# Kernel tuning notes

Measured on AMD Instinct MI355X. Metric: run time of the kernel, lower is better.

The kernel has to match this reference:

```python
import jax, jax.numpy as jnp
import numpy as np

B, U, D, SKIP = 2048, 1024, 1024, 24

def setup_inputs() -> dict:
    key = jax.random.key(0)
    ks = jax.random.split(key, 8)
    return {
        "inputs": jax.random.normal(ks[0], (B, D), dtype=jnp.float32),
        "h_tm1": jax.random.normal(ks[1], (B, 4 * U), dtype=jnp.float32),
        "c_tm1": jax.random.normal(ks[2], (B, U), dtype=jnp.float32),
        "step": jnp.zeros((B, 1), dtype=jnp.float32),
        "prev_h": jax.random.normal(ks[3], (B, U * SKIP), dtype=jnp.float32),
        "kernel": jax.random.normal(ks[4], (D, 4 * U), dtype=jnp.float32) * (1.0 / np.sqrt(D)),
        "recurrent_kernel": jax.random.normal(ks[5], (U, 4 * U), dtype=jnp.float32) * (1.0 / np.sqrt(U)),
        "kernel2": jax.random.normal(ks[6], (U, U), dtype=jnp.float32) * (1.0 / np.sqrt(U)),
        "bias": jnp.zeros((4 * U,), dtype=jnp.float32),
        "bias2": jnp.zeros((U,), dtype=jnp.float32),
        "s0": jnp.float32(0.5),
    }

def reference(inputs, h_tm1, c_tm1, step, prev_h, kernel, recurrent_kernel, kernel2, bias, bias2, s0):
    units = kernel2.shape[0]
    # split previous 'h' state into its four gate-history blocks [B, U] each
    h_parts = jnp.stack(jnp.split(h_tm1, 4, axis=1), axis=0)          # [4, B, U]
    rk = recurrent_kernel.reshape(units, 4, units)                     # [U, 4, U]
    # fused per-gate recurrent matmuls: r[g] = h_parts[g] @ recurrent_kernel[:, g*U:(g+1)*U]
    r = jnp.einsum('gbu,ugv->gbv', h_parts, rk)                        # [4, B, U]
    x = inputs @ kernel + bias                                         # [B, 4U]
    x_i, x_f, x_c, x_o = jnp.split(x, 4, axis=1)
    i = jax.nn.sigmoid(x_i + r[0])
    f = jax.nn.sigmoid(x_f + r[1])
    c = f * c_tm1 + i * jnp.tanh(x_c + r[2])
    o = jax.nn.sigmoid(x_o + r[3])
    h = o * jnp.tanh(c)
    new_h_skip = jax.nn.sigmoid(prev_h[:, :units] @ kernel2 + bias2)
    h = s0 * h + new_h_skip * (1 - s0)
    new_h_tm1 = jnp.concatenate([i, f, c, o], axis=1)
    new_prev_h = jnp.concatenate([prev_h[:, units:], h], axis=1)
    return (h, new_h_tm1, c, step + 1, new_prev_h)
```

## Files before the change

### kernel.cpp

```cpp
#include <hip/hip_runtime.h>
#include <hip/hip_bf16.h>
#include <stdint.h>

#define BB 2048
#define UU 1024
#define SKIPN 24

typedef __attribute__((ext_vector_type(8))) short short8;
typedef __attribute__((ext_vector_type(4))) float f32x4;
typedef __attribute__((ext_vector_type(4))) unsigned short ushort4_t;

static __device__ __forceinline__ float sigmoidf_(float x) {
    return 1.0f / (1.0f + __expf(-x));
}

static __device__ __forceinline__ void load_lds16(const void* g, void* l) {
    __builtin_amdgcn_global_load_lds((const __attribute__((address_space(1))) void*)g,
                                     (__attribute__((address_space(3))) void*)l, 16, 0, 0);
}

__global__ __launch_bounds__(256) void transpose_all(
    const float* __restrict__ w0, const float* __restrict__ w1,
    const float* __restrict__ w2, __hip_bfloat16* __restrict__ kt,
    __hip_bfloat16* __restrict__ rkt, __hip_bfloat16* __restrict__ k2t) {
    const int z = blockIdx.z;
    const float* src = (z == 0) ? w0 : (z == 1) ? w1 : w2;
    __hip_bfloat16* dst = (z == 0) ? kt : (z == 1) ? rkt : k2t;
    const int C = (z == 2) ? 1024 : 4096;
    const int bc = blockIdx.x * 32;
    if (bc >= C) return;
    const int br = blockIdx.y * 32;
    __shared__ float tile[32][33];
    const int tx = threadIdx.x & 31;
    const int ty = threadIdx.x >> 5;
#pragma unroll
    for (int i = 0; i < 32; i += 8)
        tile[ty + i][tx] = src[(size_t)(br + ty + i) * C + bc + tx];
    __syncthreads();
#pragma unroll
    for (int i = 0; i < 32; i += 8)
        dst[(size_t)(bc + ty + i) * 1024 + br + tx] = __float2bfloat16(tile[tx][ty + i]);
}

__global__ __launch_bounds__(256) void convert_all(
    const float* __restrict__ inputs, const float* __restrict__ h_tm1,
    const float* __restrict__ prev_h, __hip_bfloat16* __restrict__ xin_bf,
    __hip_bfloat16* __restrict__ h_bf, __hip_bfloat16* __restrict__ ph0_bf) {
    const int idx = blockIdx.x * 256 + threadIdx.x;
    const float* src;
    __hip_bfloat16* dst;
    int off;
    if (idx < 524288) {
        src = inputs; dst = xin_bf; off = idx;
        src += (size_t)off * 4;
    } else if (idx < 2621440) {
        off = idx - 524288; dst = h_bf;
        src = h_tm1 + (size_t)off * 4;
    } else {
        const int i = idx - 2621440;
        const int b = i >> 8, c4 = i & 255;
        off = i; dst = ph0_bf;
        src = prev_h + (size_t)b * (UU * SKIPN) + c4 * 4;
    }
    const float4 v = *(const float4*)src;
    union { __hip_bfloat16 h[4]; ushort4_t u; } cv;
    cv.h[0] = __float2bfloat16(v.x);
    cv.h[1] = __float2bfloat16(v.y);
    cv.h[2] = __float2bfloat16(v.z);
    cv.h[3] = __float2bfloat16(v.w);
    *(ushort4_t*)(dst + (size_t)off * 4) = cv.u;
}

__global__ __launch_bounds__(256) void gemm128(
    const __hip_bfloat16* __restrict__ xin_bf,
    const __hip_bfloat16* __restrict__ h_bf,
    const __hip_bfloat16* __restrict__ ph0_bf,
    const __hip_bfloat16* __restrict__ kt,
    const __hip_bfloat16* __restrict__ rkt,
    const __hip_bfloat16* __restrict__ k2t,
    float* __restrict__ pre) {
    __shared__ short As[128 * 32];
    __shared__ short Bs[128 * 32];

    const int tid = threadIdx.x;
    const int lane = tid & 63;
    const int wid = tid >> 6;
    const int wrow = wid >> 1;
    const int wcol = wid & 1;
    const int g = blockIdx.z;
    const int v0 = blockIdx.x * 128;
    const int b0 = blockIdx.y * 128;

    const int srow = tid >> 2;
    const int sslot = tid & 3;
    const int kofs = ((sslot ^ (srow & 3)) << 3);
    char* dA = (char*)As + wid * 1024;
    char* dB = (char*)Bs + wid * 1024;

    const int l15 = lane & 15;
    const int hi = lane >> 4;
    const int rswB = ((hi ^ (l15 & 3)) << 4);

    f32x4 acc[4][4];
#pragma unroll
    for (int m = 0; m < 4; m++)
#pragma unroll
        for (int n = 0; n < 4; n++) acc[m][n] = (f32x4){0.f, 0.f, 0.f, 0.f};

    const __hip_bfloat16* A1;
    const __hip_bfloat16* W1;
    const __hip_bfloat16* A2 = nullptr;
    const __hip_bfloat16* W2 = nullptr;
    int lda1;
    if (g < 4) {
        A1 = xin_bf; lda1 = 1024;
        W1 = kt + (size_t)g * 1048576;
        A2 = h_bf + (size_t)g * 1024;
        W2 = rkt + (size_t)g * 1048576;
    } else {
        A1 = ph0_bf; lda1 = 1024;
        W1 = k2t;
    }

#define KSEG(AB, LDA, WB)                                                          \
    {                                                                              \
        const __hip_bfloat16* Ar0 = (AB) + (size_t)(b0 + srow) * (LDA) + kofs;     \
        const __hip_bfloat16* Ar1 = (AB) + (size_t)(b0 + 64 + srow) * (LDA) + kofs;\
        const __hip_bfloat16* Wr0 = (WB) + (size_t)(v0 + srow) * 1024 + kofs;      \
        const __hip_bfloat16* Wr1 = (WB) + (size_t)(v0 + 64 + srow) * 1024 + kofs; \
        for (int k0 = 0; k0 < 1024; k0 += 32) {                                    \
            load_lds16(Ar0 + k0, dA);                                              \
            load_lds16(Ar1 + k0, dA + 4096);                                       \
            load_lds16(Wr0 + k0, dB);                                              \
            load_lds16(Wr1 + k0, dB + 4096);                                       \
            __syncthreads();                                                       \
            short8 af[4], bf[4];                                                   \
            _Pragma("unroll")                                                      \
            for (int m = 0; m < 4; m++)                                            \
                af[m] = *(const short8*)((char*)As + (wrow * 64 + m * 16 + l15) * 64 + rswB); \
            _Pragma("unroll")                                                      \
            for (int n = 0; n < 4; n++)                                            \
                bf[n] = *(const short8*)((char*)Bs + (wcol * 64 + n * 16 + l15) * 64 + rswB); \
            _Pragma("unroll")                                                      \
            for (int m = 0; m < 4; m++)                                            \
                _Pragma("unroll")                                                  \
                for (int n = 0; n < 4; n++)                                        \
                    acc[m][n] = __builtin_amdgcn_mfma_f32_16x16x32_bf16(af[m], bf[n], acc[m][n], 0, 0, 0); \
            __syncthreads();                                                       \
        }                                                                          \
    }

    KSEG(A1, lda1, W1);
    if (g < 4) KSEG(A2, 4096, W2);
#undef KSEG

    float* P = pre + (size_t)g * 2097152;
#pragma unroll
    for (int m = 0; m < 4; m++) {
#pragma unroll
        for (int n = 0; n < 4; n++) {
            const int col = v0 + wcol * 64 + n * 16 + l15;
            const int row = b0 + wrow * 64 + m * 16 + hi * 4;
#pragma unroll
            for (int r = 0; r < 4; r++)
                P[(size_t)(row + r) * 1024 + col] = acc[m][n][r];
        }
    }
}

__global__ __launch_bounds__(256) void epilogue(
    const float* __restrict__ pre,
    const float* __restrict__ c_tm1, const float* __restrict__ bias,
    const float* __restrict__ bias2, const float* __restrict__ s0p,
    float* __restrict__ out_h, float* __restrict__ out_ht, float* __restrict__ out_c) {
    const int idx = blockIdx.x * 256 + threadIdx.x;
    const int b = idx >> 8;
    const int v = (idx & 255) * 4;
    const size_t bv = (size_t)b * 1024 + v;
    const float4 pi = *(const float4*)(pre + bv);
    const float4 pf = *(const float4*)(pre + 2097152 + bv);
    const float4 pc = *(const float4*)(pre + 4194304 + bv);
    const float4 po = *(const float4*)(pre + 6291456 + bv);
    const float4 ps = *(const float4*)(pre + 8388608 + bv);
    const float4 ct = *(const float4*)(c_tm1 + bv);
    const float4 bi = *(const float4*)(bias + v);
    const float4 bf_ = *(const float4*)(bias + 1024 + v);
    const float4 bc = *(const float4*)(bias + 2048 + v);
    const float4 bo = *(const float4*)(bias + 3072 + v);
    const float4 b2 = *(const float4*)(bias2 + v);
    const float s0 = s0p[0];

    float4 hv, iv4, fv4, cn4, ov4;
#pragma unroll
    for (int j = 0; j < 4; j++) {
        const float iv = sigmoidf_(((const float*)&pi)[j] + ((const float*)&bi)[j]);
        const float fv = sigmoidf_(((const float*)&pf)[j] + ((const float*)&bf_)[j]);
        const float cn = fv * ((const float*)&ct)[j] + iv * tanhf(((const float*)&pc)[j] + ((const float*)&bc)[j]);
        const float ov = sigmoidf_(((const float*)&po)[j] + ((const float*)&bo)[j]);
        const float sk = sigmoidf_(((const float*)&ps)[j] + ((const float*)&b2)[j]);
        ((float*)&hv)[j] = s0 * (ov * tanhf(cn)) + sk * (1.0f - s0);
        ((float*)&iv4)[j] = iv;
        ((float*)&fv4)[j] = fv;
        ((float*)&cn4)[j] = cn;
        ((float*)&ov4)[j] = ov;
    }
    *(float4*)(out_h + bv) = hv;
    *(float4*)(out_c + bv) = cn4;
    float* ht = out_ht + (size_t)b * 4096 + v;
    *(float4*)(ht) = iv4;
    *(float4*)(ht + 1024) = fv4;
    *(float4*)(ht + 2048) = cn4;
    *(float4*)(ht + 3072) = ov4;
}

__global__ __launch_bounds__(256) void copy_shift(
    const float* __restrict__ prev_h, const float* __restrict__ out_h,
    const float* __restrict__ step, float* __restrict__ out_prev,
    float* __restrict__ out_step) {
    const int C4 = (UU * SKIPN) / 4;
    int idx = blockIdx.x * 256 + threadIdx.x;
    if (idx >= BB * C4) return;
    int b = idx / C4;
    int c4 = idx - b * C4;
    int col = c4 * 4;
    float4 v;
    if (col < UU * (SKIPN - 1))
        v = *(const float4*)(prev_h + (size_t)b * (UU * SKIPN) + col + UU);
    else
        v = *(const float4*)(out_h + (size_t)b * UU + (col - UU * (SKIPN - 1)));
    *(float4*)(out_prev + (size_t)b * (UU * SKIPN) + col) = v;
    if (idx < BB) out_step[idx] = step[idx] + 1.0f;
}

extern "C" void kernel_launch(void* const* d_in, const int* in_sizes, int n_in,
                              void* d_out, int out_size, void* d_ws, size_t ws_size,
                              hipStream_t stream) {
    (void)in_sizes; (void)n_in; (void)out_size; (void)d_ws; (void)ws_size;
    const float* inputs = (const float*)d_in[0];
    const float* h_tm1 = (const float*)d_in[1];
    const float* c_tm1 = (const float*)d_in[2];
    const float* step = (const float*)d_in[3];
    const float* prev_h = (const float*)d_in[4];
    const float* kernel = (const float*)d_in[5];
    const float* rkernel = (const float*)d_in[6];
    const float* kernel2 = (const float*)d_in[7];
    const float* bias = (const float*)d_in[8];
    const float* bias2 = (const float*)d_in[9];
    const float* s0 = (const float*)d_in[10];

    float* out = (float*)d_out;
    float* out_h = out;
    float* out_ht = out + 2097152;
    float* out_c = out + 10485760;
    float* out_step = out + 12582912;
    float* out_prev = out + 12584960;

    char* scr = (char*)out_prev;
    __hip_bfloat16* kt = (__hip_bfloat16*)(scr + 0);
    __hip_bfloat16* rkt = (__hip_bfloat16*)(scr + 8388608);
    __hip_bfloat16* k2t = (__hip_bfloat16*)(scr + 16777216);
    __hip_bfloat16* xin_bf = (__hip_bfloat16*)(scr + 18874368);
    __hip_bfloat16* h_bf = (__hip_bfloat16*)(scr + 23068672);
    __hip_bfloat16* ph0_bf = (__hip_bfloat16*)(scr + 39845888);
    float* pre = (float*)(scr + 44040192);

    transpose_all<<<dim3(128, 32, 3), 256, 0, stream>>>(kernel, rkernel, kernel2, kt, rkt, k2t);
    convert_all<<<12288, 256, 0, stream>>>(inputs, h_tm1, prev_h, xin_bf, h_bf, ph0_bf);
    gemm128<<<dim3(8, 16, 5), 256, 0, stream>>>(xin_bf, h_bf, ph0_bf, kt, rkt, k2t, pre);
    epilogue<<<2048, 256, 0, stream>>>(pre, c_tm1, bias, bias2, s0, out_h, out_ht, out_c);
    copy_shift<<<(BB * 6144 + 255) / 256, 256, 0, stream>>>(prev_h, out_h, step, out_prev, out_step);
}
```

Measured before the change: 190.1 us.

## Fuse prep kernels and overlap prev_h shift copy with GEMM blocks

Merges the weight transpose and activation conversion into one prep launch. When the workspace is large enough, scratch moves out of the output buffer, so the large prev_h shift copy can run inside the GEMM launch as extra blocks (one in six), overlapping memory-bound copy with MFMA compute. The tail write of h and the step increment move into the epilogue, removing a separate copy kernel. The copy blocks take CU slots from GEMM tiles, and a fallback path keeps the old ordering when the workspace is too small.

```diff
diff --git a/kernel.cpp b/kernel.cpp
--- a/kernel.cpp
+++ b/kernel.cpp
@@ -19,66 +19,88 @@
                                      (__attribute__((address_space(3))) void*)l, 16, 0, 0);
 }
 
-__global__ __launch_bounds__(256) void transpose_all(
-    const float* __restrict__ w0, const float* __restrict__ w1,
-    const float* __restrict__ w2, __hip_bfloat16* __restrict__ kt,
-    __hip_bfloat16* __restrict__ rkt, __hip_bfloat16* __restrict__ k2t) {
-    const int z = blockIdx.z;
-    const float* src = (z == 0) ? w0 : (z == 1) ? w1 : w2;
-    __hip_bfloat16* dst = (z == 0) ? kt : (z == 1) ? rkt : k2t;
-    const int C = (z == 2) ? 1024 : 4096;
-    const int bc = blockIdx.x * 32;
-    if (bc >= C) return;
-    const int br = blockIdx.y * 32;
-    __shared__ float tile[32][33];
-    const int tx = threadIdx.x & 31;
-    const int ty = threadIdx.x >> 5;
-#pragma unroll
-    for (int i = 0; i < 32; i += 8)
-        tile[ty + i][tx] = src[(size_t)(br + ty + i) * C + bc + tx];
-    __syncthreads();
-#pragma unroll
-    for (int i = 0; i < 32; i += 8)
-        dst[(size_t)(bc + ty + i) * 1024 + br + tx] = __float2bfloat16(tile[tx][ty + i]);
-}
-
-__global__ __launch_bounds__(256) void convert_all(
+__global__ __launch_bounds__(256) void prep(
     const float* __restrict__ inputs, const float* __restrict__ h_tm1,
-    const float* __restrict__ prev_h, __hip_bfloat16* __restrict__ xin_bf,
-    __hip_bfloat16* __restrict__ h_bf, __hip_bfloat16* __restrict__ ph0_bf) {
-    const int idx = blockIdx.x * 256 + threadIdx.x;
-    const float* src;
-    __hip_bfloat16* dst;
-    int off;
-    if (idx < 524288) {
-        src = inputs; dst = xin_bf; off = idx;
-        src += (size_t)off * 4;
-    } else if (idx < 2621440) {
-        off = idx - 524288; dst = h_bf;
-        src = h_tm1 + (size_t)off * 4;
+    const float* __restrict__ prev_h, const float* __restrict__ kernel,
+    const float* __restrict__ rkernel, const float* __restrict__ kernel2,
+    __hip_bfloat16* __restrict__ kt, __hip_bfloat16* __restrict__ rkt,
+    __hip_bfloat16* __restrict__ k2t, __hip_bfloat16* __restrict__ xin,
+    __hip_bfloat16* __restrict__ hb, __hip_bfloat16* __restrict__ ph0) {
+    const int bid = blockIdx.x;
+    if (bid < 9216) {
+        __shared__ float tile[32][33];
+        const float* src;
+        __hip_bfloat16* dst;
+        int C, local;
+        if (bid < 4096)      { src = kernel;  dst = kt;  C = 4096; local = bid; }
+        else if (bid < 8192) { src = rkernel; dst = rkt; C = 4096; local = bid - 4096; }
+        else                 { src = kernel2; dst = k2t; C = 1024; local = bid - 8192; }
+        const int xt = (C == 4096) ? 128 : 32;
+        const int bc = (local % xt) * 32;
+        const int br = (local / xt) * 32;
+        const int tx = threadIdx.x & 31, ty = threadIdx.x >> 5;
+#pragma unroll
+        for (int i = 0; i < 32; i += 8)
+            tile[ty + i][tx] = src[(size_t)(br + ty + i) * C + bc + tx];
+        __syncthreads();
+#pragma unroll
+        for (int i = 0; i < 32; i += 8)
+            dst[(size_t)(bc + ty + i) * 1024 + br + tx] = __float2bfloat16(tile[tx][ty + i]);
     } else {
-        const int i = idx - 2621440;
-        const int b = i >> 8, c4 = i & 255;
-        off = i; dst = ph0_bf;
-        src = prev_h + (size_t)b * (UU * SKIPN) + c4 * 4;
-    }
-    const float4 v = *(const float4*)src;
-    union { __hip_bfloat16 h[4]; ushort4_t u; } cv;
-    cv.h[0] = __float2bfloat16(v.x);
-    cv.h[1] = __float2bfloat16(v.y);
-    cv.h[2] = __float2bfloat16(v.z);
-    cv.h[3] = __float2bfloat16(v.w);
-    *(ushort4_t*)(dst + (size_t)off * 4) = cv.u;
-}
-
-__global__ __launch_bounds__(256) void gemm128(
-    const __hip_bfloat16* __restrict__ xin_bf,
-    const __hip_bfloat16* __restrict__ h_bf,
-    const __hip_bfloat16* __restrict__ ph0_bf,
+        const int idx = (bid - 9216) * 256 + threadIdx.x;
+        const float* src;
+        __hip_bfloat16* dst;
+        int off;
+        if (idx < 524288) { dst = xin; off = idx; src = inputs + (size_t)off * 4; }
+        else if (idx < 2621440) { off = idx - 524288; dst = hb; src = h_tm1 + (size_t)off * 4; }
+        else {
+            const int i = idx - 2621440;
+            const int b = i >> 8, c4 = i & 255;
+            off = i; dst = ph0;
+            src = prev_h + (size_t)b * (UU * SKIPN) + c4 * 4;
+        }
+        const float4 v = *(const float4*)src;
+        union { __hip_bfloat16 h[4]; ushort4_t u; } cv;
+        cv.h[0] = __float2bfloat16(v.x);
+        cv.h[1] = __float2bfloat16(v.y);
+        cv.h[2] = __float2bfloat16(v.z);
+        cv.h[3] = __float2bfloat16(v.w);
+        *(ushort4_t*)(dst + (size_t)off * 4) = cv.u;
+    }
+}
+
+__global__ __launch_bounds__(256) void mega2(
+    const __hip_bfloat16* __restrict__ xin,
+    const __hip_bfloat16* __restrict__ hb,
+    const __hip_bfloat16* __restrict__ ph0,
     const __hip_bfloat16* __restrict__ kt,
     const __hip_bfloat16* __restrict__ rkt,
     const __hip_bfloat16* __restrict__ k2t,
-    float* __restrict__ pre) {
+    const float* __restrict__ prev_h, float* __restrict__ out_prev,
+    float* __restrict__ pre,
+    int do_copy) {
+    const int bid = blockIdx.x;
+    int gi;
+    if (do_copy) {
+        const int q = bid / 6, r = bid - q * 6;
+        if (r == 5) {
+            for (int rr = 0; rr < 16; ++rr) {
+                const int b = q * 16 + rr;
+                const float4* s = (const float4*)(prev_h + (size_t)b * 24576 + 1024);
+                float4* d = (float4*)(out_prev + (size_t)b * 24576);
+                for (int c = threadIdx.x; c < 5888; c += 256) d[c] = s[c];
+            }
+            return;
+        }
+        gi = q * 5 + r;
+    } else {
+        gi = bid;
+    }
+    const int g = gi % 5;
+    const int t = gi / 5;
+    const int v0 = (t & 7) * 128;
+    const int b0 = (t >> 3) * 128;
+
     __shared__ short As[128 * 32];
     __shared__ short Bs[128 * 32];
 
@@ -87,9 +109,6 @@
     const int wid = tid >> 6;
     const int wrow = wid >> 1;
     const int wcol = wid & 1;
-    const int g = blockIdx.z;
-    const int v0 = blockIdx.x * 128;
-    const int b0 = blockIdx.y * 128;
 
     const int srow = tid >> 2;
     const int sslot = tid & 3;
@@ -113,12 +132,12 @@
     const __hip_bfloat16* W2 = nullptr;
     int lda1;
     if (g < 4) {
-        A1 = xin_bf; lda1 = 1024;
+        A1 = xin; lda1 = 1024;
         W1 = kt + (size_t)g * 1048576;
-        A2 = h_bf + (size_t)g * 1024;
+        A2 = hb + (size_t)g * 1024;
         W2 = rkt + (size_t)g * 1048576;
     } else {
-        A1 = ph0_bf; lda1 = 1024;
+        A1 = ph0; lda1 = 1024;
         W1 = k2t;
     }
 
@@ -134,18 +153,18 @@
             load_lds16(Wr0 + k0, dB);                                              \
             load_lds16(Wr1 + k0, dB + 4096);                                       \
             __syncthreads();                                                       \
-            short8 af[4], bf[4];                                                   \
+            short8 af[4], bfr[4];                                                  \
             _Pragma("unroll")                                                      \
             for (int m = 0; m < 4; m++)                                            \
                 af[m] = *(const short8*)((char*)As + (wrow * 64 + m * 16 + l15) * 64 + rswB); \
             _Pragma("unroll")                                                      \
             for (int n = 0; n < 4; n++)                                            \
-                bf[n] = *(const short8*)((char*)Bs + (wcol * 64 + n * 16 + l15) * 64 + rswB); \
+                bfr[n] = *(const short8*)((char*)Bs + (wcol * 64 + n * 16 + l15) * 64 + rswB); \
             _Pragma("unroll")                                                      \
             for (int m = 0; m < 4; m++)                                            \
                 _Pragma("unroll")                                                  \
                 for (int n = 0; n < 4; n++)                                        \
-                    acc[m][n] = __builtin_amdgcn_mfma_f32_16x16x32_bf16(af[m], bf[n], acc[m][n], 0, 0, 0); \
+                    acc[m][n] = __builtin_amdgcn_mfma_f32_16x16x32_bf16(af[m], bfr[n], acc[m][n], 0, 0, 0); \
             __syncthreads();                                                       \
         }                                                                          \
     }
@@ -168,11 +187,13 @@
     }
 }
 
-__global__ __launch_bounds__(256) void epilogue(
+__global__ __launch_bounds__(256) void epilogue2(
     const float* __restrict__ pre,
     const float* __restrict__ c_tm1, const float* __restrict__ bias,
     const float* __restrict__ bias2, const float* __restrict__ s0p,
-    float* __restrict__ out_h, float* __restrict__ out_ht, float* __restrict__ out_c) {
+    const float* __restrict__ step, float* __restrict__ out_h,
+    float* __restrict__ out_ht, float* __restrict__ out_c,
+    float* __restrict__ out_step, float* __restrict__ out_prev, int write_tail) {
     const int idx = blockIdx.x * 256 + threadIdx.x;
     const int b = idx >> 8;
     const int v = (idx & 255) * 4;
@@ -211,31 +232,29 @@
     *(float4*)(ht + 1024) = fv4;
     *(float4*)(ht + 2048) = cn4;
     *(float4*)(ht + 3072) = ov4;
-}
-
-__global__ __launch_bounds__(256) void copy_shift(
+    if (write_tail)
+        *(float4*)(out_prev + (size_t)b * 24576 + 23552 + v) = hv;
+    if (idx < 2048) out_step[idx] = step[idx] + 1.0f;
+}
+
+__global__ __launch_bounds__(512) void shift_only(
     const float* __restrict__ prev_h, const float* __restrict__ out_h,
-    const float* __restrict__ step, float* __restrict__ out_prev,
-    float* __restrict__ out_step) {
-    const int C4 = (UU * SKIPN) / 4;
-    int idx = blockIdx.x * 256 + threadIdx.x;
-    if (idx >= BB * C4) return;
-    int b = idx / C4;
-    int c4 = idx - b * C4;
-    int col = c4 * 4;
-    float4 v;
-    if (col < UU * (SKIPN - 1))
-        v = *(const float4*)(prev_h + (size_t)b * (UU * SKIPN) + col + UU);
-    else
-        v = *(const float4*)(out_h + (size_t)b * UU + (col - UU * (SKIPN - 1)));
-    *(float4*)(out_prev + (size_t)b * (UU * SKIPN) + col) = v;
-    if (idx < BB) out_step[idx] = step[idx] + 1.0f;
+    float* __restrict__ out_prev) {
+    const int cb = blockIdx.x;
+    for (int r = 0; r < 16; ++r) {
+        const int b = cb * 16 + r;
+        float4* d = (float4*)(out_prev + (size_t)b * 24576);
+        const float4* s1 = (const float4*)(prev_h + (size_t)b * 24576 + 1024);
+        const float4* s2 = (const float4*)(out_h + (size_t)b * 1024);
+        for (int c = threadIdx.x; c < 6144; c += 512)
+            d[c] = (c < 5888) ? s1[c] : s2[c - 5888];
+    }
 }
 
 extern "C" void kernel_launch(void* const* d_in, const int* in_sizes, int n_in,
                               void* d_out, int out_size, void* d_ws, size_t ws_size,
                               hipStream_t stream) {
-    (void)in_sizes; (void)n_in; (void)out_size; (void)d_ws; (void)ws_size;
+    (void)in_sizes; (void)n_in; (void)out_size;
     const float* inputs = (const float*)d_in[0];
     const float* h_tm1 = (const float*)d_in[1];
     const float* c_tm1 = (const float*)d_in[2];
@@ -255,18 +274,27 @@
     float* out_step = out + 12582912;
     float* out_prev = out + 12584960;
 
-    char* scr = (char*)out_prev;
+    const size_t NEED = 44040192 + 41943040;
+    const int fits = (ws_size >= NEED);
+    char* scr = fits ? (char*)d_ws : (char*)out_prev;
     __hip_bfloat16* kt = (__hip_bfloat16*)(scr + 0);
     __hip_bfloat16* rkt = (__hip_bfloat16*)(scr + 8388608);
     __hip_bfloat16* k2t = (__hip_bfloat16*)(scr + 16777216);
-    __hip_bfloat16* xin_bf = (__hip_bfloat16*)(scr + 18874368);
-    __hip_bfloat16* h_bf = (__hip_bfloat16*)(scr + 23068672);
-    __hip_bfloat16* ph0_bf = (__hip_bfloat16*)(scr + 39845888);
+    __hip_bfloat16* xin = (__hip_bfloat16*)(scr + 18874368);
+    __hip_bfloat16* hb = (__hip_bfloat16*)(scr + 23068672);
+    __hip_bfloat16* ph0 = (__hip_bfloat16*)(scr + 39845888);
     float* pre = (float*)(scr + 44040192);
 
-    transpose_all<<<dim3(128, 32, 3), 256, 0, stream>>>(kernel, rkernel, kernel2, kt, rkt, k2t);
-    convert_all<<<12288, 256, 0, stream>>>(inputs, h_tm1, prev_h, xin_bf, h_bf, ph0_bf);
-    gemm128<<<dim3(8, 16, 5), 256, 0, stream>>>(xin_bf, h_bf, ph0_bf, kt, rkt, k2t, pre);
-    epilogue<<<2048, 256, 0, stream>>>(pre, c_tm1, bias, bias2, s0, out_h, out_ht, out_c);
-    copy_shift<<<(BB * 6144 + 255) / 256, 256, 0, stream>>>(prev_h, out_h, step, out_prev, out_step);
-}
+    prep<<<21504, 256, 0, stream>>>(inputs, h_tm1, prev_h, kernel, rkernel, kernel2,
+                                    kt, rkt, k2t, xin, hb, ph0);
+    if (fits) {
+        mega2<<<768, 256, 0, stream>>>(xin, hb, ph0, kt, rkt, k2t, prev_h, out_prev, pre, 1);
+        epilogue2<<<2048, 256, 0, stream>>>(pre, c_tm1, bias, bias2, s0, step,
+                                            out_h, out_ht, out_c, out_step, out_prev, 1);
+    } else {
+        mega2<<<640, 256, 0, stream>>>(xin, hb, ph0, kt, rkt, k2t, prev_h, out_prev, pre, 0);
+        epilogue2<<<2048, 256, 0, stream>>>(pre, c_tm1, bias, bias2, s0, step,
+                                            out_h, out_ht, out_c, out_step, out_prev, 0);
+        shift_only<<<128, 512, 0, stream>>>(prev_h, out_h, out_prev);
+    }
+}
```

Result: slower. 335.7 us (+76.6%).
